# Optimization experiments

Measured on AMD Instinct MI355X. Metric: run time of the kernel, lower is better.

Reference implementation:

```python
import jax, jax.numpy as jnp
import numpy as np

BN_EPS = 1e-5
DIST_EPS = 1e-8


def setup_inputs() -> dict:
    key = jax.random.key(0)
    ks = jax.random.split(key, 8)
    B, N, S = 8, 8192, 2048
    D_unk, D_kn = 128, 256
    inp = {
        "unknown_xyz": jax.random.uniform(ks[0], (B, N, 3), dtype=jnp.float32),
        "known_xyz": jax.random.uniform(ks[1], (B, S, 3), dtype=jnp.float32),
        "unknown_points": jax.random.normal(ks[2], (B, N, D_unk), dtype=jnp.float32),
        "known_points": jax.random.normal(ks[3], (B, S, D_kn), dtype=jnp.float32),
        "W0": jax.random.normal(ks[4], (256, 384), dtype=jnp.float32) * (1.0 / np.sqrt(384)),
        "b0": jnp.zeros((256,), jnp.float32),
        "g0": jnp.ones((256,), jnp.float32),
        "beta0": jnp.zeros((256,), jnp.float32),
        "W1": jax.random.normal(ks[5], (128, 256), dtype=jnp.float32) * (1.0 / np.sqrt(256)),
        "b1": jnp.zeros((128,), jnp.float32),
        "g1": jnp.ones((128,), jnp.float32),
        "beta1": jnp.zeros((128,), jnp.float32),
    }
    return inp


def _three_nn(unknown_xyz, known_xyz):
    # squared pairwise distances [B, N, S]
    d = jnp.sum((unknown_xyz[:, :, None, :] - known_xyz[:, None, :, :]) ** 2, axis=-1)
    neg_top, idx = jax.lax.top_k(-d, 3)  # 3 smallest distances
    return -neg_top, idx  # dists [B,N,3], idx [B,N,3]


def _conv_bn_relu(x, W, b, g, beta):
    # x: [B, N, Cin]; 1x1 Conv1d == per-point linear
    y = jnp.einsum("bnc,oc->bno", x, W) + b
    mean = jnp.mean(y, axis=(0, 1))
    var = jnp.var(y, axis=(0, 1))  # biased, as BatchNorm training forward
    y = g * (y - mean) * jax.lax.rsqrt(var + BN_EPS) + beta
    return jax.nn.relu(y)


def reference(unknown_xyz, known_xyz, unknown_points, known_points,
              W0, b0, g0, beta0, W1, b1, g1, beta1):
    dists, idx = _three_nn(unknown_xyz, known_xyz)
    dist_recip = 1.0 / (dists + DIST_EPS)
    weight = dist_recip / jnp.sum(dist_recip, axis=2, keepdims=True)  # [B,N,3]
    # gather 3 neighbor features: [B,N,3,D_kn]
    gathered = jax.vmap(lambda f, i: f[i])(known_points, idx)
    interpolated = jnp.sum(weight[..., None] * gathered, axis=2)  # [B,N,D_kn]
    x = jnp.concatenate([unknown_points, interpolated], axis=-1)  # [B,N,384]
    x = _conv_bn_relu(x, W0, b0, g0, beta0)
    x = _conv_bn_relu(x, W1, b1, g1, beta1)
    return x  # [B, N, 128]
```

## Files before the change

kernel.cpp:

```cpp
#include <hip/hip_runtime.h>
#include <hip/hip_bf16.h>


typedef __attribute__((ext_vector_type(8))) short short8;
typedef __attribute__((ext_vector_type(4))) float f32x4;

#define BB 8
#define NN 8192
#define SS 2048
#define M_TOT (BB * NN)
#define N1DIM 256
#define K2DIM 256
#define N2DIM 128
#define BK 64

#define GDIM 5
#define NCELL (GDIM * GDIM * GDIM)
#define SLOTS 32
#define CELLW 0.2f

#define KEY_MASK 0xFFFFF800u
#define IDX_MASK 0x7FFu

__device__ __forceinline__ unsigned short f2bf(float f) {
    unsigned int x = __float_as_uint(f);
    unsigned int r = x + 0x7fffu + ((x >> 16) & 1u);
    return (unsigned short)(r >> 16);
}
__device__ __forceinline__ float bf2f(unsigned short u) {
    return __uint_as_float(((unsigned int)u) << 16);
}
__device__ __forceinline__ unsigned int med3_u32(unsigned int a, unsigned int b,
                                                 unsigned int c) {
    unsigned int r;
    asm("v_med3_u32 %0, %1, %2, %3" : "=v"(r) : "v"(a), "v"(b), "v"(c));
    return r;
}

__device__ __forceinline__ void ins5(unsigned int k[5], unsigned int key) {
    unsigned int n1 = med3_u32(k[0], k[1], key);
    unsigned int n2 = med3_u32(k[1], k[2], key);
    unsigned int n3 = med3_u32(k[2], k[3], key);
    unsigned int n4 = med3_u32(k[3], k[4], key);
    k[0] = min(k[0], key);
    k[1] = n1; k[2] = n2; k[3] = n3; k[4] = n4;
}

__device__ __forceinline__ float rescue_write(
    const unsigned int k[5], float qx, float qy, float qz,
    const float4* __restrict__ kpB, uint4* __restrict__ widx, size_t pt)
{
    unsigned long long e[5];
#pragma unroll
    for (int i = 0; i < 5; ++i) {
        if ((k[i] & KEY_MASK) >= 0x7F800000u) {
            e[i] = 0xFFFFFFFFFFFFFFFFull;
        } else {
            unsigned int idx = k[i] & IDX_MASK;
            float4 c = kpB[idx];
            float dx = c.x - qx, dy = c.y - qy, dz = c.z - qz;
            float d = fmaf(dx, dx, fmaf(dy, dy, dz * dz));
            e[i] = ((unsigned long long)__float_as_uint(d) << 32) | idx;
        }
    }
#pragma unroll
    for (int i = 0; i < 3; ++i)
#pragma unroll
        for (int j = i + 1; j < 5; ++j)
            if (e[j] < e[i]) { unsigned long long t = e[i]; e[i] = e[j]; e[j] = t; }

    float d0 = __uint_as_float((unsigned int)(e[0] >> 32));
    float d1 = __uint_as_float((unsigned int)(e[1] >> 32));
    float d2 = __uint_as_float((unsigned int)(e[2] >> 32));
    float r0 = 1.0f / (d0 + 1e-8f);
    float r1 = 1.0f / (d1 + 1e-8f);
    float r2 = 1.0f / (d2 + 1e-8f);
    float rs = 1.0f / (r0 + r1 + r2);
    unsigned int i0 = (unsigned int)(e[0] & IDX_MASK);
    unsigned int i1 = (unsigned int)(e[1] & IDX_MASK);
    unsigned int i2 = (unsigned int)(e[2] & IDX_MASK);
    widx[pt] = make_uint4(__float_as_uint(r0 * rs), __float_as_uint(r1 * rs),
                          i0 | (i1 << 16), i2);
    return d2;
}

__device__ __forceinline__ void gload_lds16(const void* g, void* lds) {
    __builtin_amdgcn_global_load_lds(
        (const __attribute__((address_space(1))) unsigned int*)g,
        (__attribute__((address_space(3))) unsigned int*)lds, 16, 0, 0);
}

__global__ __launch_bounds__(256) void cvt_w_kernel(
    const float* __restrict__ W0, const float* __restrict__ W1,
    const float* __restrict__ kxyz,
    unsigned short* __restrict__ Wa, unsigned short* __restrict__ Wb,
    unsigned short* __restrict__ Wb1, float4* __restrict__ kpack,
    float4* __restrict__ table, int* __restrict__ cnt,
    int* __restrict__ nfail, float* __restrict__ statsF)
{
    int i = blockIdx.x * 256 + threadIdx.x;
    if (blockIdx.x == 0) {
        for (int j = threadIdx.x; j < 4608; j += 256) statsF[j] = 0.0f;
        if (threadIdx.x == 0) *nfail = 0;
    }
    if (i < BB * NCELL) cnt[i] = 0;
    if (i < BB * NCELL * SLOTS)
        table[i] = make_float4(1e30f, 1e30f, 1e30f, 0.0f);
    if (i < 256 * 384) {
        int o = i / 384, c = i - o * 384;
        unsigned short v = f2bf(W0[i]);
        if (c < 128) Wa[o * 128 + c] = v;
        else         Wb[o * 256 + (c - 128)] = v;
    }
    if (i < N2DIM * K2DIM) Wb1[i] = f2bf(W1[i]);
    if (i < BB * SS) {
        const float* p = kxyz + (size_t)i * 3;
        float px = p[0], py = p[1], pz = p[2];
        kpack[i] = make_float4(px, py, pz, fmaf(px, px, fmaf(py, py, pz * pz)));
    }
}

__global__ __launch_bounds__(256) void bin_scatter_kernel(
    const float* __restrict__ kxyz, float4* __restrict__ table,
    int* __restrict__ cnt)
{
    int i = blockIdx.x * 256 + threadIdx.x;
    if (i >= BB * SS) return;
    int b = i >> 11, s = i & 2047;
    const float* p = kxyz + (size_t)i * 3;
    float x = p[0], y = p[1], z = p[2];
    int cx = min((int)(x * GDIM), GDIM - 1);
    int cy = min((int)(y * GDIM), GDIM - 1);
    int cz = min((int)(z * GDIM), GDIM - 1);
    int cell = (cz * GDIM + cy) * GDIM + cx;
    int slot = atomicAdd(&cnt[b * NCELL + cell], 1);
    if (slot < SLOTS)
        table[((size_t)(b * NCELL + cell)) * SLOTS + slot] =
            make_float4(x, y, z, __int_as_float(s));
}

#define NNB 512
#define ZB  256
#define G1B 1024
__global__ __launch_bounds__(512, 4) void mid_kernel(
    const float* __restrict__ uxyz, const float4* __restrict__ table,
    const int* __restrict__ cnt, const float4* __restrict__ kpack,
    uint4* __restrict__ widx, int* __restrict__ fail_list,
    int* __restrict__ nfail,
    const float* __restrict__ kpts, const unsigned short* __restrict__ Wb,
    unsigned short* __restrict__ Z,
    const float* __restrict__ upts, const unsigned short* __restrict__ Wa,
    unsigned short* __restrict__ Y0u)
{
    __shared__ __align__(128) unsigned char smem[65536];
    const int bid = blockIdx.x;
    const int tid = threadIdx.x;

    if (bid < NNB) {
        const int t  = bid * 512 + tid;
        const int qd = t & 3;
        const size_t pt = (size_t)(t >> 2);
        const int b = (int)(pt >> 13);

        const float* up = uxyz + pt * 3;
        const float qx = up[0], qy = up[1], qz = up[2];

        const int cx = min((int)(qx * GDIM), GDIM - 1);
        const int cy = min((int)(qy * GDIM), GDIM - 1);
        const int cz = min((int)(qz * GDIM), GDIM - 1);
        const float fx = qx * GDIM - cx, fy = qy * GDIM - cy, fz = qz * GDIM - cz;
        int ox = cx - (fx <= 0.5f ? 1 : 0); ox = max(0, min(ox, GDIM - 2));
        int oy = cy - (fy <= 0.5f ? 1 : 0); oy = max(0, min(oy, GDIM - 2));
        int oz = cz - (fz <= 0.5f ? 1 : 0); oz = max(0, min(oz, GDIM - 2));

        const float4* tb = table + (size_t)b * NCELL * SLOTS;
        const int* cb = cnt + b * NCELL;

        unsigned int k[5] = {0xFFFFFFFFu, 0xFFFFFFFFu, 0xFFFFFFFFu,
                             0xFFFFFFFFu, 0xFFFFFFFFu};
        int ovf = 0;
#pragma unroll
        for (int jj = 0; jj < 2; ++jj) {
            const int j = qd * 2 + jj;
            const int dx = j & 1, dy = (j >> 1) & 1, dz = j >> 2;
            const int cell = ((oz + dz) * GDIM + (oy + dy)) * GDIM + (ox + dx);
            ovf |= (cb[cell] > SLOTS) ? 1 : 0;
            const float4* cp = tb + (size_t)cell * SLOTS;
#pragma unroll 8
            for (int s = 0; s < SLOTS; ++s) {
                float4 c = cp[s];
                float ddx = c.x - qx, ddy = c.y - qy, ddz = c.z - qz;
                float d = fmaf(ddx, ddx, fmaf(ddy, ddy, ddz * ddz));
                unsigned int key = (__float_as_uint(d) & KEY_MASK) |
                                   (unsigned int)__float_as_int(c.w);
                ins5(k, key);
            }
        }

#pragma unroll
        for (int m = 1; m <= 2; m <<= 1) {
            unsigned int f0 = (unsigned int)__shfl_xor((int)k[0], m);
            unsigned int f1 = (unsigned int)__shfl_xor((int)k[1], m);
            unsigned int f2 = (unsigned int)__shfl_xor((int)k[2], m);
            unsigned int f3 = (unsigned int)__shfl_xor((int)k[3], m);
            unsigned int f4 = (unsigned int)__shfl_xor((int)k[4], m);
            ovf |= __shfl_xor(ovf, m);
            ins5(k, f0); ins5(k, f1); ins5(k, f2); ins5(k, f3); ins5(k, f4);
        }

        if (qd != 0) return;

        float d3 = rescue_write(k, qx, qy, qz, kpack + (size_t)b * SS, widx, pt);

        float lx = ox * CELLW, rx = (ox + 2) * CELLW;
        float ly = oy * CELLW, ry = (oy + 2) * CELLW;
        float lz = oz * CELLW, rz = (oz + 2) * CELLW;
        float covx = fminf(ox == 0 ? 1e30f : qx - lx, ox == GDIM - 2 ? 1e30f : rx - qx);
        float covy = fminf(oy == 0 ? 1e30f : qy - ly, oy == GDIM - 2 ? 1e30f : ry - qy);
        float covz = fminf(oz == 0 ? 1e30f : qz - lz, oz == GDIM - 2 ? 1e30f : rz - qz);
        float g = fminf(covx, fminf(covy, covz));

        if (ovf || !(d3 <= g * g)) {
            int pos = atomicAdd(nfail, 1);
            fail_list[pos] = (int)pt;
        }
        return;
    }

    const int l = tid & 63, w = tid >> 6;
    const int wm = w >> 2, wn = w & 3;
    const int srow = l >> 3, sbo = (l & 7) * 16;
    const int lr = tid >> 2, lcq = tid & 3;

    if (bid < NNB + ZB) {
        const int vb = bid - NNB;
        const int mt = vb >> 1, nh = vb & 1;
        const int row0 = mt * 128;

        f32x4 acc[4][2];
#pragma unroll
        for (int m = 0; m < 4; ++m)
#pragma unroll
            for (int n = 0; n < 2; ++n) {
                f32x4 z = {0.f, 0.f, 0.f, 0.f};
                acc[m][n] = z;
            }

        const unsigned char* Bb = (const unsigned char*)Wb + (size_t)nh * 128 * 512;
        float4 af0, af1, af2, af3;

        auto issueA = [&](int t) {
            const float* src = kpts + (size_t)(row0 + lr) * 256 + t * 64 + lcq * 16;
            af0 = ((const float4*)src)[0];
            af1 = ((const float4*)src)[1];
            af2 = ((const float4*)src)[2];
            af3 = ((const float4*)src)[3];
        };
        auto stageB = [&](int buf, int t) {
            unsigned char* Bl = smem + buf * 32768 + 16384;
#pragma unroll
            for (int i = 0; i < 2; ++i) {
                const int r = w * 16 + i * 8 + srow;
                gload_lds16(Bb + (size_t)r * 512 + t * 128 + (sbo ^ ((r & 7) << 4)),
                            Bl + r * 128 + sbo);
            }
        };
        auto xformA = [&](int buf) {
            unsigned char* Al = smem + buf * 32768;
            short8 o0, o1;
            o0[0] = (short)f2bf(af0.x); o0[1] = (short)f2bf(af0.y);
            o0[2] = (short)f2bf(af0.z); o0[3] = (short)f2bf(af0.w);
            o0[4] = (short)f2bf(af1.x); o0[5] = (short)f2bf(af1.y);
            o0[6] = (short)f2bf(af1.z); o0[7] = (short)f2bf(af1.w);
            o1[0] = (short)f2bf(af2.x); o1[1] = (short)f2bf(af2.y);
            o1[2] = (short)f2bf(af2.z); o1[3] = (short)f2bf(af2.w);
            o1[4] = (short)f2bf(af3.x); o1[5] = (short)f2bf(af3.y);
            o1[6] = (short)f2bf(af3.z); o1[7] = (short)f2bf(af3.w);
            const int bo = lcq * 32;
            *(short8*)(Al + lr * 128 + ((bo) ^ ((lr & 7) << 4))) = o0;
            *(short8*)(Al + lr * 128 + ((bo + 16) ^ ((lr & 7) << 4))) = o1;
        };
        auto compute = [&](int buf) {
            const unsigned char* Al = smem + buf * 32768;
            const unsigned char* Bl = Al + 16384;
#pragma unroll
            for (int ks = 0; ks < 2; ++ks) {
                const int bo = ks * 64 + (l >> 4) * 16;
                short8 a[4], bq[2];
#pragma unroll
                for (int m = 0; m < 4; ++m) {
                    const int r = wm * 64 + m * 16 + (l & 15);
                    a[m] = *(const short8*)(Al + r * 128 + (bo ^ ((r & 7) << 4)));
                }
#pragma unroll
                for (int n = 0; n < 2; ++n) {
                    const int r = wn * 32 + n * 16 + (l & 15);
                    bq[n] = *(const short8*)(Bl + r * 128 + (bo ^ ((r & 7) << 4)));
                }
#pragma unroll
                for (int m = 0; m < 4; ++m)
#pragma unroll
                    for (int n = 0; n < 2; ++n)
                        acc[m][n] = __builtin_amdgcn_mfma_f32_16x16x32_bf16(
                            a[m], bq[n], acc[m][n], 0, 0, 0);
            }
        };

        issueA(0);
        stageB(0, 0);
        xformA(0);
        __syncthreads();
#pragma unroll
        for (int t = 0; t < 4; ++t) {
            const int cur = t & 1;
            if (t + 1 < 4) { issueA(t + 1); stageB(cur ^ 1, t + 1); }
            compute(cur);
            if (t + 1 < 4) xformA(cur ^ 1);
            __syncthreads();
        }

#pragma unroll
        for (int m = 0; m < 4; ++m) {
            const int row = row0 + wm * 64 + m * 16 + (l >> 4) * 4;
#pragma unroll
            for (int n = 0; n < 2; ++n) {
                const int col = nh * 128 + wn * 32 + n * 16 + (l & 15);
                f32x4 v = acc[m][n];
#pragma unroll
                for (int r = 0; r < 4; ++r)
                    Z[(size_t)(row + r) * 256 + col] = f2bf(v[r]);
            }
        }
        return;
    }

    {
        const int vb = bid - (NNB + ZB);
        const int mt = vb >> 1, nh = vb & 1;
        const int row0 = mt * 128;

        {
            const unsigned char* Bb = (const unsigned char*)Wa + (size_t)nh * 128 * 256;
#pragma unroll
            for (int h = 0; h < 2; ++h)
#pragma unroll
                for (int i = 0; i < 2; ++i) {
                    const int r = w * 16 + i * 8 + srow;
                    gload_lds16(Bb + (size_t)r * 256 + h * 128 + (sbo ^ ((r & 7) << 4)),
                                smem + 32768 + h * 16384 + r * 128 + sbo);
                }
        }
        {
            const float* src = upts + (size_t)(row0 + lr) * 128 + lcq * 32;
            float4 f[8];
#pragma unroll
            for (int q = 0; q < 8; ++q) f[q] = ((const float4*)src)[q];
            unsigned char* Ah = smem + (lcq >> 1) * 16384;
            const int cb = (lcq & 1) * 64;
#pragma unroll
            for (int q = 0; q < 4; ++q) {
                float4 fa = f[q * 2], fb = f[q * 2 + 1];
                short8 o;
                o[0] = (short)f2bf(fa.x); o[1] = (short)f2bf(fa.y);
                o[2] = (short)f2bf(fa.z); o[3] = (short)f2bf(fa.w);
                o[4] = (short)f2bf(fb.x); o[5] = (short)f2bf(fb.y);
                o[6] = (short)f2bf(fb.z); o[7] = (short)f2bf(fb.w);
                *(short8*)(Ah + lr * 128 + ((cb + q * 16) ^ ((lr & 7) << 4))) = o;
            }
        }
        __syncthreads();

        f32x4 acc[4][2];
#pragma unroll
        for (int m = 0; m < 4; ++m)
#pragma unroll
            for (int n = 0; n < 2; ++n) {
                f32x4 z = {0.f, 0.f, 0.f, 0.f};
                acc[m][n] = z;
            }
#pragma unroll
        for (int ks = 0; ks < 4; ++ks) {
            const unsigned char* Al = smem + (ks >> 1) * 16384;
            const unsigned char* Bl = smem + 32768 + (ks >> 1) * 16384;
            const int bo = (ks & 1) * 64 + (l >> 4) * 16;
            short8 a[4], bq[2];
#pragma unroll
            for (int m = 0; m < 4; ++m) {
                const int r = wm * 64 + m * 16 + (l & 15);
                a[m] = *(const short8*)(Al + r * 128 + (bo ^ ((r & 7) << 4)));
            }
#pragma unroll
            for (int n = 0; n < 2; ++n) {
                const int r = wn * 32 + n * 16 + (l & 15);
                bq[n] = *(const short8*)(Bl + r * 128 + (bo ^ ((r & 7) << 4)));
            }
#pragma unroll
            for (int m = 0; m < 4; ++m)
#pragma unroll
                for (int n = 0; n < 2; ++n)
                    acc[m][n] = __builtin_amdgcn_mfma_f32_16x16x32_bf16(
                        a[m], bq[n], acc[m][n], 0, 0, 0);
        }

        __syncthreads();
        {
            unsigned short* st = (unsigned short*)smem;
#pragma unroll
            for (int m = 0; m < 4; ++m)
#pragma unroll
                for (int n = 0; n < 2; ++n)
#pragma unroll
                    for (int r = 0; r < 4; ++r) {
                        const int row = wm * 64 + m * 16 + (l >> 4) * 4 + r;
                        const int col = wn * 32 + n * 16 + (l & 15);
                        st[row * 136 + col] = f2bf(acc[m][n][r]);
                    }
        }
        __syncthreads();
        {
            const int row = tid >> 2, cb = (tid & 3) * 32;
            const unsigned short* st = (const unsigned short*)smem;
            unsigned short* dst = Y0u + (size_t)(row0 + row) * 256 + nh * 128 + cb;
#pragma unroll
            for (int i = 0; i < 4; ++i)
                *(short8*)(dst + i * 8) = *(const short8*)(st + row * 136 + cb + i * 8);
        }
    }
}

__global__ __launch_bounds__(256) void nn_brute_kernel(
    const float* __restrict__ uxyz, const float4* __restrict__ kpack,
    const int* __restrict__ fail_list, const int* __restrict__ nfail,
    uint4* __restrict__ widx)
{
    const int l = threadIdx.x & 63;
    const int wv = (blockIdx.x * 256 + threadIdx.x) >> 6;
    const int nw = (gridDim.x * 256) >> 6;
    const int n = *nfail;

    for (int q = wv; q < n; q += nw) {
        const size_t pt = (size_t)fail_list[q];
        const int b = (int)(pt >> 13);
        const float* up = uxyz + pt * 3;
        const float qx = up[0], qy = up[1], qz = up[2];
        const float4* kp = kpack + (size_t)b * SS;

        unsigned int k[5] = {0xFFFFFFFFu, 0xFFFFFFFFu, 0xFFFFFFFFu,
                             0xFFFFFFFFu, 0xFFFFFFFFu};
#pragma unroll 4
        for (int s = l; s < SS; s += 64) {
            float4 c = kp[s];
            float ddx = c.x - qx, ddy = c.y - qy, ddz = c.z - qz;
            float d = fmaf(ddx, ddx, fmaf(ddy, ddy, ddz * ddz));
            unsigned int key = (__float_as_uint(d) & KEY_MASK) | (unsigned int)s;
            ins5(k, key);
        }
#pragma unroll
        for (int m = 1; m <= 32; m <<= 1) {
            unsigned int f0 = (unsigned int)__shfl_xor((int)k[0], m);
            unsigned int f1 = (unsigned int)__shfl_xor((int)k[1], m);
            unsigned int f2 = (unsigned int)__shfl_xor((int)k[2], m);
            unsigned int f3 = (unsigned int)__shfl_xor((int)k[3], m);
            unsigned int f4 = (unsigned int)__shfl_xor((int)k[4], m);
            ins5(k, f0); ins5(k, f1); ins5(k, f2); ins5(k, f3); ins5(k, f4);
        }
        if (l == 0)
            rescue_write(k, qx, qy, qz, kp, widx, pt);
    }
}

__global__ __launch_bounds__(256) void interp_y0_kernel(
    const uint4* __restrict__ widx,
    const unsigned short* __restrict__ Z,
    const unsigned short* __restrict__ Y0u,
    unsigned short* __restrict__ Y0,
    float* __restrict__ statsR)
{
    __shared__ int   sidx[64][3];
    __shared__ float sw[64][3];
    __shared__ float sst[4][512];

    const int tid = threadIdx.x;
    const int bid = blockIdx.x;
    const int b   = bid & 7;
    const int pn  = (bid >> 3) * 64;
    const int wv = tid >> 6, lane = tid & 63;

    if (tid < 64) {
        uint4 wq = widx[(size_t)b * NN + pn + tid];
        float w0 = __uint_as_float(wq.x);
        float w1 = __uint_as_float(wq.y);
        sidx[tid][0] = (int)(wq.z & 0xFFFFu);
        sidx[tid][1] = (int)(wq.z >> 16);
        sidx[tid][2] = (int)wq.w;
        sw[tid][0] = w0; sw[tid][1] = w1; sw[tid][2] = 1.0f - w0 - w1;
    }
    __syncthreads();

    float s1[4] = {0.f, 0.f, 0.f, 0.f}, s2[4] = {0.f, 0.f, 0.f, 0.f};
    const unsigned short* Zb = Z + (size_t)b * SS * 256;
    for (int p = wv; p < 64; p += 4) {
        const int j0 = sidx[p][0], j1 = sidx[p][1], j2 = sidx[p][2];
        const float w0 = sw[p][0], w1 = sw[p][1], w2 = sw[p][2];
        const size_t rb = ((size_t)b * NN + pn + p) * 256 + lane * 4;

        ushort4 z0 = *(const ushort4*)(Zb + (size_t)j0 * 256 + lane * 4);
        ushort4 z1 = *(const ushort4*)(Zb + (size_t)j1 * 256 + lane * 4);
        ushort4 z2 = *(const ushort4*)(Zb + (size_t)j2 * 256 + lane * 4);
        ushort4 u  = *(const ushort4*)(Y0u + rb);

        float f0 = bf2f(u.x) + fmaf(w2, bf2f(z2.x), fmaf(w1, bf2f(z1.x), w0 * bf2f(z0.x)));
        float f1 = bf2f(u.y) + fmaf(w2, bf2f(z2.y), fmaf(w1, bf2f(z1.y), w0 * bf2f(z0.y)));
        float f2v = bf2f(u.z) + fmaf(w2, bf2f(z2.z), fmaf(w1, bf2f(z1.z), w0 * bf2f(z0.z)));
        float f3 = bf2f(u.w) + fmaf(w2, bf2f(z2.w), fmaf(w1, bf2f(z1.w), w0 * bf2f(z0.w)));

        ushort4 o;
        o.x = f2bf(f0); o.y = f2bf(f1); o.z = f2bf(f2v); o.w = f2bf(f3);
        *(ushort4*)(Y0 + rb) = o;

        s1[0] += f0;  s2[0] += f0 * f0;
        s1[1] += f1;  s2[1] += f1 * f1;
        s1[2] += f2v; s2[2] += f2v * f2v;
        s1[3] += f3;  s2[3] += f3 * f3;
    }

#pragma unroll
    for (int j = 0; j < 4; ++j) {
        sst[wv][lane * 4 + j] = s1[j];
        sst[wv][256 + lane * 4 + j] = s2[j];
    }
    __syncthreads();
    {
        float v = sst[0][tid] + sst[1][tid] + sst[2][tid] + sst[3][tid];
        float q = sst[0][256 + tid] + sst[1][256 + tid] +
                  sst[2][256 + tid] + sst[3][256 + tid];
        atomicAdd(&statsR[b * 512 + tid], v);
        atomicAdd(&statsR[b * 512 + 256 + tid], q);
    }
}

#define G2_NT (K2DIM / BK)
__global__ __launch_bounds__(512, 4) void gemm2_kernel(
    const unsigned short* __restrict__ Y0,
    const unsigned short* __restrict__ Wb,
    const float* __restrict__ statsR,
    const float* __restrict__ g0,
    const float* __restrict__ beta0,
    unsigned short* __restrict__ Y1,
    float* __restrict__ stats)
{
    __shared__ __align__(128) unsigned char smem[2 * 32768];
    __shared__ float sgm[K2DIM], sga[K2DIM];

    const int tid = threadIdx.x;
    const int l = tid & 63, w = tid >> 6;
    const int wm = w >> 2, wn = w & 3;
    const int row0 = blockIdx.x * 128;
    const int srow = l >> 3;
    const int sbo  = (l & 7) * 16;
    const int lr  = tid >> 2;
    const int lcq = tid & 3;

    f32x4 acc[4][2];
#pragma unroll
    for (int m = 0; m < 4; ++m)
#pragma unroll
        for (int n = 0; n < 2; ++n) {
            f32x4 z = {0.f, 0.f, 0.f, 0.f};
            acc[m][n] = z;
        }

    const unsigned char* Bb = (const unsigned char*)Wb;
    short8 areg0, areg1;

    auto issueA = [&](int t) {
        const unsigned short* src = Y0 + (size_t)(row0 + lr) * K2DIM + t * BK + lcq * 16;
        areg0 = *(const short8*)src;
        areg1 = *(const short8*)(src + 8);
    };
    auto stageB = [&](int buf, int t) {
        unsigned char* Bl = smem + buf * 32768 + 16384;
        const int k0b = t * (BK * 2);
#pragma unroll
        for (int i = 0; i < 2; ++i) {
            const int r = w * 16 + i * 8 + srow;
            gload_lds16(Bb + (size_t)r * (K2DIM * 2) + k0b + (sbo ^ ((r & 7) << 4)),
                        Bl + r * 128 + sbo);
        }
    };
    auto xformA = [&](int buf, int t) {
        unsigned char* Al = smem + buf * 32768;
        const int kb = t * BK + lcq * 16;
        short8 o0, o1;
#pragma unroll
        for (int j = 0; j < 8; ++j) {
            float f = bf2f((unsigned short)areg0[j]);
            f = fmaxf(fmaf(f, sgm[kb + j], sga[kb + j]), 0.f);
            o0[j] = (short)f2bf(f);
            float g = bf2f((unsigned short)areg1[j]);
            g = fmaxf(fmaf(g, sgm[kb + 8 + j], sga[kb + 8 + j]), 0.f);
            o1[j] = (short)f2bf(g);
        }
        const int bo = lcq * 32;
        *(short8*)(Al + lr * 128 + ((bo) ^ ((lr & 7) << 4))) = o0;
        *(short8*)(Al + lr * 128 + ((bo + 16) ^ ((lr & 7) << 4))) = o1;
    };
    auto compute = [&](int buf) {
        const unsigned char* Al = smem + buf * 32768;
        const unsigned char* Bl = Al + 16384;
#pragma unroll
        for (int ks = 0; ks < 2; ++ks) {
            const int bo = ks * 64 + (l >> 4) * 16;
            short8 a[4], bq[2];
#pragma unroll
            for (int m = 0; m < 4; ++m) {
                const int r = wm * 64 + m * 16 + (l & 15);
                a[m] = *(const short8*)(Al + r * 128 + (bo ^ ((r & 7) << 4)));
            }
#pragma unroll
            for (int n = 0; n < 2; ++n) {
                const int r = wn * 32 + n * 16 + (l & 15);
                bq[n] = *(const short8*)(Bl + r * 128 + (bo ^ ((r & 7) << 4)));
            }
#pragma unroll
            for (int m = 0; m < 4; ++m)
#pragma unroll
                for (int n = 0; n < 2; ++n)
                    acc[m][n] = __builtin_amdgcn_mfma_f32_16x16x32_bf16(
                        a[m], bq[n], acc[m][n], 0, 0, 0);
        }
    };

    if (tid < K2DIM) {
        float s = 0.f, q = 0.f;
#pragma unroll
        for (int r = 0; r < 8; ++r) {
            s += statsR[r * 512 + tid];
            q += statsR[r * 512 + 256 + tid];
        }
        const float inv = 1.0f / (float)M_TOT;
        float mean = s * inv;
        float var  = q * inv - mean * mean;
        float m = g0[tid] * rsqrtf(var + 1e-5f);
        sgm[tid] = m;
        sga[tid] = beta0[tid] - mean * m;
    }
    issueA(0);
    stageB(0, 0);
    __syncthreads();
    xformA(0, 0);
    __syncthreads();

#pragma unroll
    for (int t = 0; t < G2_NT; ++t) {
        const int cur = t & 1;
        if (t + 1 < G2_NT) { issueA(t + 1); stageB(cur ^ 1, t + 1); }
        compute(cur);
        if (t + 1 < G2_NT) xformA(cur ^ 1, t + 1);
        __syncthreads();
    }

    float s1[2] = {0.f, 0.f}, s2[2] = {0.f, 0.f};
#pragma unroll
    for (int m = 0; m < 4; ++m) {
        const int row = row0 + wm * 64 + m * 16 + (l >> 4) * 4;
#pragma unroll
        for (int n = 0; n < 2; ++n) {
            const int col = wn * 32 + n * 16 + (l & 15);
            f32x4 v = acc[m][n];
#pragma unroll
            for (int r = 0; r < 4; ++r) {
                float f = v[r];
                Y1[(size_t)(row + r) * N2DIM + col] = f2bf(f);
                s1[n] += f;
                s2[n] += f * f;
            }
        }
    }
#pragma unroll
    for (int n = 0; n < 2; ++n) {
        s1[n] += __shfl_xor(s1[n], 16, 64);
        s1[n] += __shfl_xor(s1[n], 32, 64);
        s2[n] += __shfl_xor(s2[n], 16, 64);
        s2[n] += __shfl_xor(s2[n], 32, 64);
    }
    if (l < 16) {
#pragma unroll
        for (int n = 0; n < 2; ++n) {
            const int col = wn * 32 + n * 16 + l;
            atomicAdd(&stats[col], s1[n]);
            atomicAdd(&stats[N2DIM + col], s2[n]);
        }
    }
}

__global__ __launch_bounds__(256) void bn_out_kernel(
    const unsigned short* __restrict__ Y1, const float* __restrict__ stats1,
    const float* __restrict__ g1, const float* __restrict__ beta1,
    float* __restrict__ out)
{
    __shared__ float sgm[N2DIM], sga[N2DIM];
    const int tid = threadIdx.x;
    if (tid < N2DIM) {
        const float inv = 1.0f / (float)M_TOT;
        float mean = stats1[tid] * inv;
        float var  = stats1[N2DIM + tid] * inv - mean * mean;
        float m = g1[tid] * rsqrtf(var + 1e-5f);
        sgm[tid] = m;
        sga[tid] = beta1[tid] - mean * m;
    }
    __syncthreads();

    const int total = M_TOT * N2DIM / 8;
    for (int i = blockIdx.x * 256 + tid; i < total; i += gridDim.x * 256) {
        short8 v = ((const short8*)Y1)[i];
        const int cg = (i & 15) * 8;
        float4 o1, o2;
        o1.x = fmaxf(fmaf(bf2f((unsigned short)v[0]), sgm[cg + 0], sga[cg + 0]), 0.f);
        o1.y = fmaxf(fmaf(bf2f((unsigned short)v[1]), sgm[cg + 1], sga[cg + 1]), 0.f);
        o1.z = fmaxf(fmaf(bf2f((unsigned short)v[2]), sgm[cg + 2], sga[cg + 2]), 0.f);
        o1.w = fmaxf(fmaf(bf2f((unsigned short)v[3]), sgm[cg + 3], sga[cg + 3]), 0.f);
        o2.x = fmaxf(fmaf(bf2f((unsigned short)v[4]), sgm[cg + 4], sga[cg + 4]), 0.f);
        o2.y = fmaxf(fmaf(bf2f((unsigned short)v[5]), sgm[cg + 5], sga[cg + 5]), 0.f);
        o2.z = fmaxf(fmaf(bf2f((unsigned short)v[6]), sgm[cg + 6], sga[cg + 6]), 0.f);
        o2.w = fmaxf(fmaf(bf2f((unsigned short)v[7]), sgm[cg + 7], sga[cg + 7]), 0.f);
        ((float4*)out)[i * 2]     = o1;
        ((float4*)out)[i * 2 + 1] = o2;
    }
}

extern "C" void kernel_launch(void* const* d_in, const int* in_sizes, int n_in,
                              void* d_out, int out_size, void* d_ws, size_t ws_size,
                              hipStream_t stream)
{
    const float* uxyz  = (const float*)d_in[0];
    const float* kxyz  = (const float*)d_in[1];
    const float* upts  = (const float*)d_in[2];
    const float* kpts  = (const float*)d_in[3];
    const float* W0    = (const float*)d_in[4];
    const float* g0    = (const float*)d_in[6];
    const float* beta0 = (const float*)d_in[7];
    const float* W1    = (const float*)d_in[8];
    const float* g1    = (const float*)d_in[10];
    const float* beta1 = (const float*)d_in[11];
    float* out = (float*)d_out;

    char* ws = (char*)d_ws;
    const size_t off_xz = 0;
    const size_t off_y0 = 33554432;
    const size_t off_z  = 67108864;
    const size_t off_w  = 75497472;

    unsigned short* Y0u  = (unsigned short*)(ws + off_xz);
    unsigned short* y1   = (unsigned short*)(ws + off_xz);
    unsigned short* y0   = (unsigned short*)(ws + off_y0);
    float4* table    = (float4*)(ws + off_y0);
    int*    cellcnt  = (int*)(ws + off_y0 + 524288);
    int*    nfail    = (int*)(ws + off_y0 + 528384);
    int*    faillist = (int*)(ws + off_y0 + 532480);
    float4* kpack    = (float4*)(ws + off_y0 + 8388608);
    unsigned short* Zb   = (unsigned short*)(ws + off_z);
    unsigned short* wa   = (unsigned short*)(ws + off_w);
    unsigned short* wb   = (unsigned short*)(ws + off_w + 65536);
    unsigned short* wb1  = (unsigned short*)(ws + off_w + 196608);
    float* F = (float*)(ws + off_w + 262144);
    float* statsR = F;
    float* stats1 = F + 4096;
    uint4* widx = (uint4*)(ws + off_w + 262144 + 18432);

    cvt_w_kernel<<<384, 256, 0, stream>>>(W0, W1, kxyz, wa, wb, wb1, kpack,
                                          table, cellcnt, nfail, F);
    bin_scatter_kernel<<<64, 256, 0, stream>>>(kxyz, table, cellcnt);
    mid_kernel<<<NNB + ZB + G1B, 512, 0, stream>>>(
        uxyz, table, cellcnt, kpack, widx, faillist, nfail,
        kpts, wb, Zb, upts, wa, Y0u);
    nn_brute_kernel<<<64, 256, 0, stream>>>(uxyz, kpack, faillist, nfail, widx);
    interp_y0_kernel<<<1024, 256, 0, stream>>>(widx, Zb, Y0u, y0, statsR);
    gemm2_kernel<<<512, 512, 0, stream>>>(y0, wb1, statsR, g0, beta0, y1, stats1);
    bn_out_kernel<<<2048, 256, 0, stream>>>(y1, stats1, g1, beta1, out);
}
```

Measured before the change: 145.2 us.

## Halve mid_kernel LDS and interleave NN, Z and GEMM1 blocks across grid

Cuts mid_kernel shared memory from 64KB to 32KB and raises launch bounds to 8 waves per SIMD so more blocks can be resident per CU. The Z GEMM drops its double-buffered pipeline for a single-buffer loop, and GEMM1 streams its K halves through the same buffer and writes its output in two 64-row halves. Blocks are interleaved in groups of 7 (2 NN, 1 Z, 4 GEMM1) so the latency-bound search work and the MFMA work share CUs at the same time. In exchange the GEMM paths gain extra barriers and lose load/compute overlap, and the tighter register budget may cause spills.

```diff
diff --git a/kernel.cpp b/kernel.cpp
--- a/kernel.cpp
+++ b/kernel.cpp
@@ -139,10 +139,7 @@
             make_float4(x, y, z, __int_as_float(s));
 }
 
-#define NNB 512
-#define ZB  256
-#define G1B 1024
-__global__ __launch_bounds__(512, 4) void mid_kernel(
+__global__ __launch_bounds__(512, 8) void mid_kernel(
     const float* __restrict__ uxyz, const float4* __restrict__ table,
     const int* __restrict__ cnt, const float4* __restrict__ kpack,
     uint4* __restrict__ widx, int* __restrict__ fail_list,
@@ -152,12 +149,13 @@
     const float* __restrict__ upts, const unsigned short* __restrict__ Wa,
     unsigned short* __restrict__ Y0u)
 {
-    __shared__ __align__(128) unsigned char smem[65536];
+    __shared__ __align__(128) unsigned char smem[32768];
     const int bid = blockIdx.x;
     const int tid = threadIdx.x;
-
-    if (bid < NNB) {
-        const int t  = bid * 512 + tid;
+    const int r7 = bid % 7, g7 = bid / 7;
+
+    if (r7 < 2) {
+        const int t  = (g7 * 2 + r7) * 512 + tid;
         const int qd = t & 3;
         const size_t pt = (size_t)(t >> 2);
         const int b = (int)(pt >> 13);
@@ -232,9 +230,8 @@
     const int srow = l >> 3, sbo = (l & 7) * 16;
     const int lr = tid >> 2, lcq = tid & 3;
 
-    if (bid < NNB + ZB) {
-        const int vb = bid - NNB;
-        const int mt = vb >> 1, nh = vb & 1;
+    if (r7 == 2) {
+        const int mt = g7 >> 1, nh = g7 & 1;
         const int row0 = mt * 128;
 
         f32x4 acc[4][2];
@@ -249,40 +246,37 @@
         const unsigned char* Bb = (const unsigned char*)Wb + (size_t)nh * 128 * 512;
         float4 af0, af1, af2, af3;
 
-        auto issueA = [&](int t) {
-            const float* src = kpts + (size_t)(row0 + lr) * 256 + t * 64 + lcq * 16;
-            af0 = ((const float4*)src)[0];
-            af1 = ((const float4*)src)[1];
-            af2 = ((const float4*)src)[2];
-            af3 = ((const float4*)src)[3];
-        };
-        auto stageB = [&](int buf, int t) {
-            unsigned char* Bl = smem + buf * 32768 + 16384;
+#pragma unroll
+        for (int t = 0; t < 4; ++t) {
+            if (t) __syncthreads();
+            {
+                const float* src = kpts + (size_t)(row0 + lr) * 256 + t * 64 + lcq * 16;
+                af0 = ((const float4*)src)[0];
+                af1 = ((const float4*)src)[1];
+                af2 = ((const float4*)src)[2];
+                af3 = ((const float4*)src)[3];
+            }
 #pragma unroll
             for (int i = 0; i < 2; ++i) {
                 const int r = w * 16 + i * 8 + srow;
                 gload_lds16(Bb + (size_t)r * 512 + t * 128 + (sbo ^ ((r & 7) << 4)),
-                            Bl + r * 128 + sbo);
-            }
-        };
-        auto xformA = [&](int buf) {
-            unsigned char* Al = smem + buf * 32768;
-            short8 o0, o1;
-            o0[0] = (short)f2bf(af0.x); o0[1] = (short)f2bf(af0.y);
-            o0[2] = (short)f2bf(af0.z); o0[3] = (short)f2bf(af0.w);
-            o0[4] = (short)f2bf(af1.x); o0[5] = (short)f2bf(af1.y);
-            o0[6] = (short)f2bf(af1.z); o0[7] = (short)f2bf(af1.w);
-            o1[0] = (short)f2bf(af2.x); o1[1] = (short)f2bf(af2.y);
-            o1[2] = (short)f2bf(af2.z); o1[3] = (short)f2bf(af2.w);
-            o1[4] = (short)f2bf(af3.x); o1[5] = (short)f2bf(af3.y);
-            o1[6] = (short)f2bf(af3.z); o1[7] = (short)f2bf(af3.w);
-            const int bo = lcq * 32;
-            *(short8*)(Al + lr * 128 + ((bo) ^ ((lr & 7) << 4))) = o0;
-            *(short8*)(Al + lr * 128 + ((bo + 16) ^ ((lr & 7) << 4))) = o1;
-        };
-        auto compute = [&](int buf) {
-            const unsigned char* Al = smem + buf * 32768;
-            const unsigned char* Bl = Al + 16384;
+                            smem + 16384 + r * 128 + sbo);
+            }
+            {
+                short8 o0, o1;
+                o0[0] = (short)f2bf(af0.x); o0[1] = (short)f2bf(af0.y);
+                o0[2] = (short)f2bf(af0.z); o0[3] = (short)f2bf(af0.w);
+                o0[4] = (short)f2bf(af1.x); o0[5] = (short)f2bf(af1.y);
+                o0[6] = (short)f2bf(af1.z); o0[7] = (short)f2bf(af1.w);
+                o1[0] = (short)f2bf(af2.x); o1[1] = (short)f2bf(af2.y);
+                o1[2] = (short)f2bf(af2.z); o1[3] = (short)f2bf(af2.w);
+                o1[4] = (short)f2bf(af3.x); o1[5] = (short)f2bf(af3.y);
+                o1[6] = (short)f2bf(af3.z); o1[7] = (short)f2bf(af3.w);
+                const int bo = lcq * 32;
+                *(short8*)(smem + lr * 128 + ((bo) ^ ((lr & 7) << 4))) = o0;
+                *(short8*)(smem + lr * 128 + ((bo + 16) ^ ((lr & 7) << 4))) = o1;
+            }
+            __syncthreads();
 #pragma unroll
             for (int ks = 0; ks < 2; ++ks) {
                 const int bo = ks * 64 + (l >> 4) * 16;
@@ -290,12 +284,12 @@
 #pragma unroll
                 for (int m = 0; m < 4; ++m) {
                     const int r = wm * 64 + m * 16 + (l & 15);
-                    a[m] = *(const short8*)(Al + r * 128 + (bo ^ ((r & 7) << 4)));
+                    a[m] = *(const short8*)(smem + r * 128 + (bo ^ ((r & 7) << 4)));
                 }
 #pragma unroll
                 for (int n = 0; n < 2; ++n) {
                     const int r = wn * 32 + n * 16 + (l & 15);
-                    bq[n] = *(const short8*)(Bl + r * 128 + (bo ^ ((r & 7) << 4)));
+                    bq[n] = *(const short8*)(smem + 16384 + r * 128 + (bo ^ ((r & 7) << 4)));
                 }
 #pragma unroll
                 for (int m = 0; m < 4; ++m)
@@ -304,19 +298,6 @@
                         acc[m][n] = __builtin_amdgcn_mfma_f32_16x16x32_bf16(
                             a[m], bq[n], acc[m][n], 0, 0, 0);
             }
-        };
-
-        issueA(0);
-        stageB(0, 0);
-        xformA(0);
-        __syncthreads();
-#pragma unroll
-        for (int t = 0; t < 4; ++t) {
-            const int cur = t & 1;
-            if (t + 1 < 4) { issueA(t + 1); stageB(cur ^ 1, t + 1); }
-            compute(cur);
-            if (t + 1 < 4) xformA(cur ^ 1);
-            __syncthreads();
         }
 
 #pragma unroll
@@ -335,40 +316,9 @@
     }
 
     {
-        const int vb = bid - (NNB + ZB);
+        const int vb = g7 * 4 + (r7 - 3);
         const int mt = vb >> 1, nh = vb & 1;
         const int row0 = mt * 128;
-
-        {
-            const unsigned char* Bb = (const unsigned char*)Wa + (size_t)nh * 128 * 256;
-#pragma unroll
-            for (int h = 0; h < 2; ++h)
-#pragma unroll
-                for (int i = 0; i < 2; ++i) {
-                    const int r = w * 16 + i * 8 + srow;
-                    gload_lds16(Bb + (size_t)r * 256 + h * 128 + (sbo ^ ((r & 7) << 4)),
-                                smem + 32768 + h * 16384 + r * 128 + sbo);
-                }
-        }
-        {
-            const float* src = upts + (size_t)(row0 + lr) * 128 + lcq * 32;
-            float4 f[8];
-#pragma unroll
-            for (int q = 0; q < 8; ++q) f[q] = ((const float4*)src)[q];
-            unsigned char* Ah = smem + (lcq >> 1) * 16384;
-            const int cb = (lcq & 1) * 64;
-#pragma unroll
-            for (int q = 0; q < 4; ++q) {
-                float4 fa = f[q * 2], fb = f[q * 2 + 1];
-                short8 o;
-                o[0] = (short)f2bf(fa.x); o[1] = (short)f2bf(fa.y);
-                o[2] = (short)f2bf(fa.z); o[3] = (short)f2bf(fa.w);
-                o[4] = (short)f2bf(fb.x); o[5] = (short)f2bf(fb.y);
-                o[6] = (short)f2bf(fb.z); o[7] = (short)f2bf(fb.w);
-                *(short8*)(Ah + lr * 128 + ((cb + q * 16) ^ ((lr & 7) << 4))) = o;
-            }
-        }
-        __syncthreads();
 
         f32x4 acc[4][2];
 #pragma unroll
@@ -378,52 +328,86 @@
                 f32x4 z = {0.f, 0.f, 0.f, 0.f};
                 acc[m][n] = z;
             }
-#pragma unroll
-        for (int ks = 0; ks < 4; ++ks) {
-            const unsigned char* Al = smem + (ks >> 1) * 16384;
-            const unsigned char* Bl = smem + 32768 + (ks >> 1) * 16384;
-            const int bo = (ks & 1) * 64 + (l >> 4) * 16;
-            short8 a[4], bq[2];
-#pragma unroll
-            for (int m = 0; m < 4; ++m) {
-                const int r = wm * 64 + m * 16 + (l & 15);
-                a[m] = *(const short8*)(Al + r * 128 + (bo ^ ((r & 7) << 4)));
-            }
-#pragma unroll
-            for (int n = 0; n < 2; ++n) {
-                const int r = wn * 32 + n * 16 + (l & 15);
-                bq[n] = *(const short8*)(Bl + r * 128 + (bo ^ ((r & 7) << 4)));
-            }
-#pragma unroll
-            for (int m = 0; m < 4; ++m)
-#pragma unroll
-                for (int n = 0; n < 2; ++n)
-                    acc[m][n] = __builtin_amdgcn_mfma_f32_16x16x32_bf16(
-                        a[m], bq[n], acc[m][n], 0, 0, 0);
-        }
-
-        __syncthreads();
-        {
-            unsigned short* st = (unsigned short*)smem;
-#pragma unroll
-            for (int m = 0; m < 4; ++m)
-#pragma unroll
-                for (int n = 0; n < 2; ++n)
-#pragma unroll
-                    for (int r = 0; r < 4; ++r) {
-                        const int row = wm * 64 + m * 16 + (l >> 4) * 4 + r;
-                        const int col = wn * 32 + n * 16 + (l & 15);
-                        st[row * 136 + col] = f2bf(acc[m][n][r]);
-                    }
-        }
-        __syncthreads();
-        {
-            const int row = tid >> 2, cb = (tid & 3) * 32;
-            const unsigned short* st = (const unsigned short*)smem;
-            unsigned short* dst = Y0u + (size_t)(row0 + row) * 256 + nh * 128 + cb;
-#pragma unroll
-            for (int i = 0; i < 4; ++i)
-                *(short8*)(dst + i * 8) = *(const short8*)(st + row * 136 + cb + i * 8);
+
+        const unsigned char* Bb = (const unsigned char*)Wa + (size_t)nh * 128 * 256;
+
+#pragma unroll
+        for (int h = 0; h < 2; ++h) {
+            if (h) __syncthreads();
+#pragma unroll
+            for (int i = 0; i < 2; ++i) {
+                const int r = w * 16 + i * 8 + srow;
+                gload_lds16(Bb + (size_t)r * 256 + h * 128 + (sbo ^ ((r & 7) << 4)),
+                            smem + 16384 + r * 128 + sbo);
+            }
+            {
+                const float* src = upts + (size_t)(row0 + lr) * 128 + h * 64 + lcq * 16;
+                float4 f0 = ((const float4*)src)[0];
+                float4 f1 = ((const float4*)src)[1];
+                float4 f2 = ((const float4*)src)[2];
+                float4 f3 = ((const float4*)src)[3];
+                short8 o0, o1;
+                o0[0] = (short)f2bf(f0.x); o0[1] = (short)f2bf(f0.y);
+                o0[2] = (short)f2bf(f0.z); o0[3] = (short)f2bf(f0.w);
+                o0[4] = (short)f2bf(f1.x); o0[5] = (short)f2bf(f1.y);
+                o0[6] = (short)f2bf(f1.z); o0[7] = (short)f2bf(f1.w);
+                o1[0] = (short)f2bf(f2.x); o1[1] = (short)f2bf(f2.y);
+                o1[2] = (short)f2bf(f2.z); o1[3] = (short)f2bf(f2.w);
+                o1[4] = (short)f2bf(f3.x); o1[5] = (short)f2bf(f3.y);
+                o1[6] = (short)f2bf(f3.z); o1[7] = (short)f2bf(f3.w);
+                const int cb = lcq * 32;
+                *(short8*)(smem + lr * 128 + ((cb) ^ ((lr & 7) << 4))) = o0;
+                *(short8*)(smem + lr * 128 + ((cb + 16) ^ ((lr & 7) << 4))) = o1;
+            }
+            __syncthreads();
+#pragma unroll
+            for (int ks = 0; ks < 2; ++ks) {
+                const int bo = ks * 64 + (l >> 4) * 16;
+                short8 a[4], bq[2];
+#pragma unroll
+                for (int m = 0; m < 4; ++m) {
+                    const int r = wm * 64 + m * 16 + (l & 15);
+                    a[m] = *(const short8*)(smem + r * 128 + (bo ^ ((r & 7) << 4)));
+                }
+#pragma unroll
+                for (int n = 0; n < 2; ++n) {
+                    const int r = wn * 32 + n * 16 + (l & 15);
+                    bq[n] = *(const short8*)(smem + 16384 + r * 128 + (bo ^ ((r & 7) << 4)));
+                }
+#pragma unroll
+                for (int m = 0; m < 4; ++m)
+#pragma unroll
+                    for (int n = 0; n < 2; ++n)
+                        acc[m][n] = __builtin_amdgcn_mfma_f32_16x16x32_bf16(
+                            a[m], bq[n], acc[m][n], 0, 0, 0);
+            }
+        }
+
+        unsigned short* st = (unsigned short*)smem;
+#pragma unroll
+        for (int h = 0; h < 2; ++h) {
+            __syncthreads();
+            if (wm == h) {
+#pragma unroll
+                for (int m = 0; m < 4; ++m)
+#pragma unroll
+                    for (int n = 0; n < 2; ++n)
+#pragma unroll
+                        for (int r = 0; r < 4; ++r) {
+                            const int rl = m * 16 + (l >> 4) * 4 + r;
+                            const int col = wn * 32 + n * 16 + (l & 15);
+                            st[rl * 136 + col] = f2bf(acc[m][n][r]);
+                        }
+            }
+            __syncthreads();
+            {
+                const int row = tid >> 3, seg = tid & 7;
+                unsigned short* dst = Y0u + (size_t)(row0 + h * 64 + row) * 256 +
+                                      nh * 128 + seg * 16;
+                const unsigned short* sp = st + row * 136 + seg * 16;
+                *(short8*)(dst)     = *(const short8*)(sp);
+                *(short8*)(dst + 8) = *(const short8*)(sp + 8);
+            }
         }
     }
 }
@@ -771,7 +755,7 @@
     cvt_w_kernel<<<384, 256, 0, stream>>>(W0, W1, kxyz, wa, wb, wb1, kpack,
                                           table, cellcnt, nfail, F);
     bin_scatter_kernel<<<64, 256, 0, stream>>>(kxyz, table, cellcnt);
-    mid_kernel<<<NNB + ZB + G1B, 512, 0, stream>>>(
+    mid_kernel<<<1792, 512, 0, stream>>>(
         uxyz, table, cellcnt, kpack, widx, faillist, nfail,
         kpts, wb, Zb, upts, wa, Y0u);
     nn_brute_kernel<<<64, 256, 0, stream>>>(uxyz, kpack, faillist, nfail, widx);
```

New measurement: 167.7 us. 15.5% more time.
